# Kernel optimization log

Hardware: AMD Instinct MI355X
Metric: run time of the kernel (lower is better)

Reference implementation:

```python
import jax, jax.numpy as jnp
import numpy as np

VOCAB = 100000
SEQ = 2048
NSYN = 4
D = 300      # embedding_size
H1 = 300     # biLSTM output dim (150 per direction)
U = 150      # LSTM units per direction


def _lstm(x, Wk, Wr, b, reverse=False):
    """Keras-style LSTM over [S, D] -> [S, U]. Gate order i, f, g(cell), o."""
    if reverse:
        x = x[::-1]
    u = Wr.shape[0]

    def step(carry, xt):
        h, c = carry
        z = xt @ Wk + h @ Wr + b              # [4U]
        i, f, g, o = jnp.split(z, 4, axis=-1)
        i = jax.nn.sigmoid(i)
        f = jax.nn.sigmoid(f)
        g = jnp.tanh(g)
        o = jax.nn.sigmoid(o)
        c = f * c + i * g
        h = o * jnp.tanh(c)
        return (h, c), h

    init = (jnp.zeros((u,), x.dtype), jnp.zeros((u,), x.dtype))
    _, hs = jax.lax.scan(step, init, x)
    return hs[::-1] if reverse else hs


def setup_inputs() -> dict:
    key = jax.random.key(0)
    ks = jax.random.split(key, 14)
    w = 0.05  # small init so exp() attention coefficients stay stable
    return {
        "sentence": jax.random.randint(ks[0], (SEQ,), 0, VOCAB),
        "synonym_indices": jax.random.randint(ks[1], (VOCAB, NSYN), 0, VOCAB),
        "embedding_matrix": jax.random.normal(ks[2], (VOCAB, D), jnp.float32) * 0.1,
        # forward LSTM
        "Wk_f": jax.random.normal(ks[3], (D, 4 * U), jnp.float32) * w,
        "Wr_f": jax.random.normal(ks[4], (U, 4 * U), jnp.float32) * w,
        "b_f": jnp.zeros((4 * U,), jnp.float32),
        # backward LSTM
        "Wk_b": jax.random.normal(ks[5], (D, 4 * U), jnp.float32) * w,
        "Wr_b": jax.random.normal(ks[6], (U, 4 * U), jnp.float32) * w,
        "b_b": jnp.zeros((4 * U,), jnp.float32),
        # primary attention dense (h1 -> h1)
        "W1": jax.random.normal(ks[7], (H1, H1), jnp.float32) * w,
        "b1": jnp.zeros((H1,), jnp.float32),
        # secondary attention dense (h1 -> 1, tanh)
        "W2": jax.random.normal(ks[8], (H1, 1), jnp.float32) * w,
        "b2": jnp.zeros((1,), jnp.float32),
        # output heads
        "We": jax.random.normal(ks[9], (H1, 8), jnp.float32) * w,
        "be": jnp.zeros((8,), jnp.float32),
        "Ws": jax.random.normal(ks[10], (H1, 1), jnp.float32) * w,
        "bs": jnp.zeros((1,), jnp.float32),
    }


def reference(sentence, synonym_indices, embedding_matrix,
              Wk_f, Wr_f, b_f, Wk_b, Wr_b, b_b,
              W1, b1, W2, b2, We, be, Ws, bs):
    emb = embedding_matrix[sentence]                       # [S, D]
    hf = _lstm(emb, Wk_f, Wr_f, b_f)                       # [S, U]
    hb = _lstm(emb, Wk_b, Wr_b, b_b, reverse=True)         # [S, U]
    hidden = jnp.concatenate([hf, hb], axis=-1)            # [S, H1]

    # ---- primary attention (vectorized over all tokens) ----
    out = hidden @ W1 + b1                                 # [S, H1]
    S = sentence.shape[0]
    # Faithful off-by-one from the original loop: token 0 uses row 0,
    # token i (i>=1) uses out/hidden row i-1.
    idx = jnp.concatenate([jnp.zeros((1,), jnp.int32),
                           jnp.arange(S - 1, dtype=jnp.int32)])
    syn_emb = embedding_matrix[synonym_indices[sentence]]  # [S, NSYN, D]
    coeff = jnp.exp(jnp.einsum('skd,sd->sk', syn_emb, out[idx]))  # [S, NSYN]
    m = jnp.einsum('sk,skd->sd', coeff, syn_emb)           # [S, D]
    h_hats = m + hidden[idx]                               # [S, H1]

    # ---- secondary attention ----
    c2 = jnp.exp(jnp.tanh(h_hats @ W2 + b2))               # [S, 1]
    H = jnp.sum(c2 * h_hats, axis=0)[None, :]              # [1, H1]

    emotion_logits = H @ We + be                           # [1, 8]
    sentiment_logits = H @ Ws + bs                         # [1, 1]
    return (emotion_logits, sentiment_logits)
```

## Files before the change

### kernel.cpp

```cpp
#include <hip/hip_runtime.h>
#include <hip/hip_bf16.h>

#define SEQ   2048
#define DIM   300
#define UU    150
#define G4    600
#define H1    300
#define NSYN  4

typedef _Float16 half2v __attribute__((ext_vector_type(2)));
union HU { unsigned u; half2v h; };

static __device__ __forceinline__ float sigm(float x) { return 1.0f / (1.0f + __expf(-x)); }
static __device__ __forceinline__ float tanh_fast(float x) { return 1.0f - 2.0f / (1.0f + __expf(2.0f * x)); }

static __device__ __forceinline__ float dot2acc(unsigned w, int h, float acc) {
    asm("v_dot2_f32_f16 %0, %1, %2, %0" : "+v"(acc) : "v"(w), "s"(h));
    return acc;
}

#define LDS_BARRIER() asm volatile("s_waitcnt lgkmcnt(0)\n\ts_barrier" ::: "memory")

__global__ void xpre_kernel(const int* __restrict__ sentence,
                            const float* __restrict__ emb_mat,
                            const float* __restrict__ Wk_f,
                            const float* __restrict__ b_f,
                            const float* __restrict__ Wk_b,
                            const float* __restrict__ b_b,
                            float* __restrict__ Xf, float* __restrict__ Xb)
{
    const int dir = blockIdx.y;
    const float* Wk = dir ? Wk_b : Wk_f;
    const float* bb = dir ? b_b : b_f;
    float* X = dir ? Xb : Xf;

    const int s0  = blockIdx.x * 8;
    const int tid = threadIdx.x;

    __shared__ int   sids[8];
    __shared__ float embs[8][DIM];

    if (tid < 8) sids[tid] = sentence[s0 + tid];
    __syncthreads();
    for (int e = tid; e < 8 * DIM; e += 640) {
        int r = e / DIM, d = e - r * DIM;
        embs[r][d] = emb_mat[(long)sids[r] * DIM + d];
    }
    __syncthreads();

    if (tid < G4) {
        float acc[8];
        float bv = bb[tid];
        #pragma unroll
        for (int r = 0; r < 8; ++r) acc[r] = bv;
        for (int k = 0; k < DIM; ++k) {
            float wv = Wk[k * G4 + tid];
            #pragma unroll
            for (int r = 0; r < 8; ++r) acc[r] = fmaf(embs[r][k], wv, acc[r]);
        }
        #pragma unroll
        for (int r = 0; r < 8; ++r) X[(long)(s0 + r) * G4 + tid] = acc[r];
    }
}

#define REP75(F) \
  F(0) F(1) F(2) F(3) F(4) F(5) F(6) F(7) F(8) F(9) \
  F(10) F(11) F(12) F(13) F(14) F(15) F(16) F(17) F(18) F(19) \
  F(20) F(21) F(22) F(23) F(24) F(25) F(26) F(27) F(28) F(29) \
  F(30) F(31) F(32) F(33) F(34) F(35) F(36) F(37) F(38) F(39) \
  F(40) F(41) F(42) F(43) F(44) F(45) F(46) F(47) F(48) F(49) \
  F(50) F(51) F(52) F(53) F(54) F(55) F(56) F(57) F(58) F(59) \
  F(60) F(61) F(62) F(63) F(64) F(65) F(66) F(67) F(68) F(69) \
  F(70) F(71) F(72) F(73) F(74)

static __device__ __forceinline__ unsigned packpair(const float* __restrict__ Wr, int c, int k) {
    HU x;
    x.h.x = (_Float16)Wr[(2 * k) * G4 + c];
    x.h.y = (_Float16)Wr[(2 * k + 1) * G4 + c];
    return x.u;
}

__global__ __launch_bounds__(256) __attribute__((amdgpu_waves_per_eu(1, 1)))
void lstm_scan_kernel(
    const float* __restrict__ Xf, const float* __restrict__ Xb,
    const float* __restrict__ Wr_f, const float* __restrict__ Wr_b,
    float* __restrict__ hidden)
{
    const int dir = blockIdx.x;
    const float* X  = dir ? Xb : Xf;
    const float* Wr = dir ? Wr_b : Wr_f;
    const int tid  = threadIdx.x;
    const int lane = tid & 63;

    __shared__ float zs[G4];
    __shared__ __align__(4) _Float16 hs16[256];

    const int c0 = tid;
    const int c1 = tid + 256;
    const bool has2 = (tid < 88);
    const int c2 = has2 ? (tid + 512) : 599;

#define WDECL(k) unsigned wA_##k, wB_##k, wC_##k;
    REP75(WDECL)
#undef WDECL
#define WLOAD(k) wA_##k = packpair(Wr, c0, k); wB_##k = packpair(Wr, c1, k); wC_##k = packpair(Wr, c2, k);
    REP75(WLOAD)
#undef WLOAD

    if (tid < 128) ((unsigned*)hs16)[tid] = 0u;
    float c = 0.0f;

    int t = dir ? (SEQ - 1) : 0;
    const int dt = dir ? -1 : 1;
    float x0 = X[t * G4 + c0];
    float x1 = X[t * G4 + c1];
    float x2 = X[t * G4 + c2];
    __syncthreads();

    const unsigned* hp = (const unsigned*)hs16;

    for (int step = 0; step < SEQ; ++step) {
        const int tn = (step < SEQ - 1) ? (t + dt) : t;
        float xn0 = X[tn * G4 + c0];
        float xn1 = X[tn * G4 + c1];
        float xn2 = X[tn * G4 + c2];

        unsigned hr0 = hp[lane];
        unsigned hr1 = hp[64 + lane];

        float a0 = x0, a1 = x1, a2 = x2;
#define DOT(k) { int hk = ((k) < 64) ? __builtin_amdgcn_readlane((int)hr0, (k)) \
                                     : __builtin_amdgcn_readlane((int)hr1, (k) - 64); \
                 a0 = dot2acc(wA_##k, hk, a0); \
                 a1 = dot2acc(wB_##k, hk, a1); \
                 a2 = dot2acc(wC_##k, hk, a2); }
        REP75(DOT)
#undef DOT

        zs[c0] = a0;
        zs[c1] = a1;
        if (has2) zs[c2] = a2;
        LDS_BARRIER();

        if (tid < UU) {
            float zi = zs[tid], zf = zs[UU + tid], zg = zs[2 * UU + tid], zo = zs[3 * UU + tid];
            float ig = sigm(zi);
            float fg = sigm(zf);
            float gg = tanh_fast(zg);
            float og = sigm(zo);
            c = fg * c + ig * gg;
            float hv = og * tanh_fast(c);
            hs16[tid] = (_Float16)hv;
            hidden[(long)t * H1 + dir * UU + tid] = hv;
        }
        LDS_BARRIER();

        x0 = xn0; x1 = xn1; x2 = xn2;
        t = tn;
    }
}

__global__ void w1_kernel(const float* __restrict__ hidden,
                          const float* __restrict__ W1,
                          const float* __restrict__ b1,
                          float* __restrict__ outm)
{
    const int s0  = blockIdx.x * 8;
    const int tid = threadIdx.x;
    __shared__ float hl[8][H1];
    for (int e = tid; e < 8 * H1; e += 320)
        hl[e / H1][e - (e / H1) * H1] = hidden[(long)s0 * H1 + e];
    __syncthreads();

    if (tid < H1) {
        float acc[8];
        float bv = b1[tid];
        #pragma unroll
        for (int r = 0; r < 8; ++r) acc[r] = bv;
        for (int k = 0; k < H1; ++k) {
            float wv = W1[k * H1 + tid];
            #pragma unroll
            for (int r = 0; r < 8; ++r) acc[r] = fmaf(hl[r][k], wv, acc[r]);
        }
        #pragma unroll
        for (int r = 0; r < 8; ++r) outm[(long)(s0 + r) * H1 + tid] = acc[r];
    }
}

static __device__ __forceinline__ float4 blockReduce4(float4 v, float* red, int tid)
{
    #pragma unroll
    for (int off = 32; off > 0; off >>= 1) {
        v.x += __shfl_down(v.x, off);
        v.y += __shfl_down(v.y, off);
        v.z += __shfl_down(v.z, off);
        v.w += __shfl_down(v.w, off);
    }
    __syncthreads();
    if ((tid & 63) == 0) {
        int wv = tid >> 6;
        red[wv * 4 + 0] = v.x; red[wv * 4 + 1] = v.y;
        red[wv * 4 + 2] = v.z; red[wv * 4 + 3] = v.w;
    }
    __syncthreads();
    float4 r;
    r.x = red[0]; r.y = red[1]; r.z = red[2]; r.w = red[3];
    #pragma unroll
    for (int wv = 1; wv < 5; ++wv) {
        r.x += red[wv * 4 + 0]; r.y += red[wv * 4 + 1];
        r.z += red[wv * 4 + 2]; r.w += red[wv * 4 + 3];
    }
    return r;
}

static __device__ __forceinline__ float blockReduce1(float v, float* red, int tid)
{
    #pragma unroll
    for (int off = 32; off > 0; off >>= 1) v += __shfl_down(v, off);
    __syncthreads();
    if ((tid & 63) == 0) red[tid >> 6] = v;
    __syncthreads();
    return red[0] + red[1] + red[2] + red[3] + red[4];
}

__global__ void attn_kernel(const int* __restrict__ sentence,
                            const int* __restrict__ syn_idx,
                            const float* __restrict__ emb_mat,
                            const float* __restrict__ outm,
                            const float* __restrict__ hidden,
                            const float* __restrict__ W2,
                            const float* __restrict__ b2,
                            float* __restrict__ whh)
{
    const int s   = blockIdx.x;
    const int t   = s ? (s - 1) : 0;
    const int tid = threadIdx.x;
    __shared__ float red[20];

    const int sent = sentence[s];
    const long i0 = (long)syn_idx[sent * NSYN + 0] * DIM;
    const long i1 = (long)syn_idx[sent * NSYN + 1] * DIM;
    const long i2 = (long)syn_idx[sent * NSYN + 2] * DIM;
    const long i3 = (long)syn_idx[sent * NSYN + 3] * DIM;

    float se0 = 0.f, se1 = 0.f, se2 = 0.f, se3 = 0.f, od = 0.f, hd = 0.f;
    if (tid < DIM) {
        se0 = emb_mat[i0 + tid];
        se1 = emb_mat[i1 + tid];
        se2 = emb_mat[i2 + tid];
        se3 = emb_mat[i3 + tid];
        od  = outm[(long)t * H1 + tid];
        hd  = hidden[(long)t * H1 + tid];
    }

    float4 dots = blockReduce4(make_float4(se0 * od, se1 * od, se2 * od, se3 * od), red, tid);
    float c0 = __expf(dots.x), c1 = __expf(dots.y), c2c = __expf(dots.z), c3 = __expf(dots.w);

    float hh = fmaf(c0, se0, fmaf(c1, se1, fmaf(c2c, se2, fmaf(c3, se3, hd))));

    float w2v = (tid < DIM) ? W2[tid] : 0.f;
    float dot2 = blockReduce1(hh * w2v, red, tid);
    float cc = __expf(tanh_fast(dot2 + b2[0]));

    if (tid < DIM) whh[(long)s * H1 + tid] = cc * hh;
}

__global__ void hred_kernel(const float* __restrict__ whh, float* __restrict__ H)
{
    const int d   = blockIdx.x;
    const int tid = threadIdx.x;
    float acc = 0.f;
    for (int s = tid; s < SEQ; s += 256) acc += whh[(long)s * H1 + d];
    #pragma unroll
    for (int off = 32; off > 0; off >>= 1) acc += __shfl_down(acc, off);
    __shared__ float red[4];
    if ((tid & 63) == 0) red[tid >> 6] = acc;
    __syncthreads();
    if (tid == 0) H[d] = red[0] + red[1] + red[2] + red[3];
}

__global__ void logits_kernel(const float* __restrict__ H,
                              const float* __restrict__ We,
                              const float* __restrict__ be,
                              const float* __restrict__ Ws,
                              const float* __restrict__ bs,
                              float* __restrict__ outp)
{
    const int e = threadIdx.x;
    if (e < 9) {
        float acc = (e < 8) ? be[e] : bs[0];
        for (int d = 0; d < H1; ++d) {
            float wv = (e < 8) ? We[d * 8 + e] : Ws[d];
            acc = fmaf(H[d], wv, acc);
        }
        outp[e] = acc;
    }
}

extern "C" void kernel_launch(void* const* d_in, const int* in_sizes, int n_in,
                              void* d_out, int out_size, void* d_ws, size_t ws_size,
                              hipStream_t stream)
{
    const int* sentence   = (const int*)d_in[0];
    const int* syn_idx    = (const int*)d_in[1];
    const float* emb      = (const float*)d_in[2];
    const float* Wk_f     = (const float*)d_in[3];
    const float* Wr_f     = (const float*)d_in[4];
    const float* b_f      = (const float*)d_in[5];
    const float* Wk_b     = (const float*)d_in[6];
    const float* Wr_b     = (const float*)d_in[7];
    const float* b_b      = (const float*)d_in[8];
    const float* W1       = (const float*)d_in[9];
    const float* b1       = (const float*)d_in[10];
    const float* W2       = (const float*)d_in[11];
    const float* b2       = (const float*)d_in[12];
    const float* We       = (const float*)d_in[13];
    const float* be       = (const float*)d_in[14];
    const float* Ws       = (const float*)d_in[15];
    const float* bs       = (const float*)d_in[16];

    float* ws     = (float*)d_ws;
    float* Xf     = ws;
    float* Xb     = Xf + (long)SEQ * G4;
    float* hidden = Xb + (long)SEQ * G4;
    float* outm   = hidden + (long)SEQ * H1;
    float* whh    = outm + (long)SEQ * H1;
    float* H      = whh + (long)SEQ * H1;

    float* outp = (float*)d_out;

    xpre_kernel<<<dim3(SEQ / 8, 2), 640, 0, stream>>>(sentence, emb, Wk_f, b_f, Wk_b, b_b, Xf, Xb);
    lstm_scan_kernel<<<2, 256, 0, stream>>>(Xf, Xb, Wr_f, Wr_b, hidden);
    w1_kernel<<<SEQ / 8, 320, 0, stream>>>(hidden, W1, b1, outm);
    attn_kernel<<<SEQ, 320, 0, stream>>>(sentence, syn_idx, emb, outm, hidden, W2, b2, whh);
    hred_kernel<<<H1, 256, 0, stream>>>(whh, H);
    logits_kernel<<<1, 64, 0, stream>>>(H, We, be, Ws, bs, outp);
}
```

Before: 2.281 ms.

## Restructure LSTM scan so each lane owns two gates and exchanges via shuffle

The recurrent scan now maps each unit to a pair of lanes in different half-waves. One lane holds the i and g gate columns and the other holds f and o, and the i*g product is passed across with a cross-lane xor shuffle. This removes the LDS round trip of the full gate vector and one of the two barriers per timestep. The previous hidden state is read from a double-buffered LDS array with 128-bit vector loads, replacing scalar readlane broadcasts, and dot-product accumulation is split across two chains for more ILP. The block grows to 320 threads and drops the one-wave-per-EU attribute, so register pressure and occupancy behavior change.

Result: slower. 2.501 ms (+9.6%).

```diff
diff --git a/kernel.cpp b/kernel.cpp
--- a/kernel.cpp
+++ b/kernel.cpp
@@ -9,13 +9,14 @@
 #define NSYN  4
 
 typedef _Float16 half2v __attribute__((ext_vector_type(2)));
+typedef unsigned u32x4 __attribute__((ext_vector_type(4)));
 union HU { unsigned u; half2v h; };
 
 static __device__ __forceinline__ float sigm(float x) { return 1.0f / (1.0f + __expf(-x)); }
 static __device__ __forceinline__ float tanh_fast(float x) { return 1.0f - 2.0f / (1.0f + __expf(2.0f * x)); }
 
-static __device__ __forceinline__ float dot2acc(unsigned w, int h, float acc) {
-    asm("v_dot2_f32_f16 %0, %1, %2, %0" : "+v"(acc) : "v"(w), "s"(h));
+static __device__ __forceinline__ float dot2v(unsigned w, unsigned h, float acc) {
+    asm("v_dot2_f32_f16 %0, %1, %2, %0" : "+v"(acc) : "v"(w), "v"(h));
     return acc;
 }
 
@@ -63,7 +64,7 @@
     }
 }
 
-#define REP75(F) \
+#define REP76(F) \
   F(0) F(1) F(2) F(3) F(4) F(5) F(6) F(7) F(8) F(9) \
   F(10) F(11) F(12) F(13) F(14) F(15) F(16) F(17) F(18) F(19) \
   F(20) F(21) F(22) F(23) F(24) F(25) F(26) F(27) F(28) F(29) \
@@ -71,16 +72,17 @@
   F(40) F(41) F(42) F(43) F(44) F(45) F(46) F(47) F(48) F(49) \
   F(50) F(51) F(52) F(53) F(54) F(55) F(56) F(57) F(58) F(59) \
   F(60) F(61) F(62) F(63) F(64) F(65) F(66) F(67) F(68) F(69) \
-  F(70) F(71) F(72) F(73) F(74)
-
-static __device__ __forceinline__ unsigned packpair(const float* __restrict__ Wr, int c, int k) {
+  F(70) F(71) F(72) F(73) F(74) F(75)
+
+static __device__ __forceinline__ unsigned packpair2(const float* __restrict__ Wr, int c, int k) {
+    if (k >= 75) return 0u;
     HU x;
     x.h.x = (_Float16)Wr[(2 * k) * G4 + c];
     x.h.y = (_Float16)Wr[(2 * k + 1) * G4 + c];
     return x.u;
 }
 
-__global__ __launch_bounds__(256) __attribute__((amdgpu_waves_per_eu(1, 1)))
+__global__ __launch_bounds__(320)
 void lstm_scan_kernel(
     const float* __restrict__ Xf, const float* __restrict__ Xb,
     const float* __restrict__ Wr_f, const float* __restrict__ Wr_b,
@@ -90,73 +92,82 @@
     const float* X  = dir ? Xb : Xf;
     const float* Wr = dir ? Wr_b : Wr_f;
     const int tid  = threadIdx.x;
-    const int lane = tid & 63;
-
-    __shared__ float zs[G4];
-    __shared__ __align__(4) _Float16 hs16[256];
-
-    const int c0 = tid;
-    const int c1 = tid + 256;
-    const bool has2 = (tid < 88);
-    const int c2 = has2 ? (tid + 512) : 599;
-
-#define WDECL(k) unsigned wA_##k, wB_##k, wC_##k;
-    REP75(WDECL)
+    const int l    = tid & 63;
+    const int w    = tid >> 6;
+    const int isB  = l >> 5;
+    const int j    = (w << 5) + (l & 31);
+    const bool active = (j < UU);
+    const int u    = active ? j : (UU - 1);
+    const int cA   = u + isB * UU;
+    const int cB   = cA + 300;
+
+    __shared__ __align__(16) unsigned hsbuf[2][80];
+
+#define WDECL(k) unsigned wA_##k, wB_##k;
+    REP76(WDECL)
 #undef WDECL
-#define WLOAD(k) wA_##k = packpair(Wr, c0, k); wB_##k = packpair(Wr, c1, k); wC_##k = packpair(Wr, c2, k);
-    REP75(WLOAD)
+#define WLOAD(k) wA_##k = packpair2(Wr, cA, k); wB_##k = packpair2(Wr, cB, k);
+    REP76(WLOAD)
 #undef WLOAD
 
-    if (tid < 128) ((unsigned*)hs16)[tid] = 0u;
+    for (int e = tid; e < 160; e += 320) ((unsigned*)hsbuf)[e] = 0u;
+
     float c = 0.0f;
-
-    int t = dir ? (SEQ - 1) : 0;
+    int tt = dir ? (SEQ - 1) : 0;
     const int dt = dir ? -1 : 1;
-    float x0 = X[t * G4 + c0];
-    float x1 = X[t * G4 + c1];
-    float x2 = X[t * G4 + c2];
-    __syncthreads();
-
-    const unsigned* hp = (const unsigned*)hs16;
+    float xA = X[(long)tt * G4 + cA];
+    float xB = X[(long)tt * G4 + cB];
+    float* hout = hidden + dir * UU + u;
+    __syncthreads();
 
     for (int step = 0; step < SEQ; ++step) {
-        const int tn = (step < SEQ - 1) ? (t + dt) : t;
-        float xn0 = X[tn * G4 + c0];
-        float xn1 = X[tn * G4 + c1];
-        float xn2 = X[tn * G4 + c2];
-
-        unsigned hr0 = hp[lane];
-        unsigned hr1 = hp[64 + lane];
-
-        float a0 = x0, a1 = x1, a2 = x2;
-#define DOT(k) { int hk = ((k) < 64) ? __builtin_amdgcn_readlane((int)hr0, (k)) \
-                                     : __builtin_amdgcn_readlane((int)hr1, (k) - 64); \
-                 a0 = dot2acc(wA_##k, hk, a0); \
-                 a1 = dot2acc(wB_##k, hk, a1); \
-                 a2 = dot2acc(wC_##k, hk, a2); }
-        REP75(DOT)
-#undef DOT
-
-        zs[c0] = a0;
-        zs[c1] = a1;
-        if (has2) zs[c2] = a2;
-        LDS_BARRIER();
-
-        if (tid < UU) {
-            float zi = zs[tid], zf = zs[UU + tid], zg = zs[2 * UU + tid], zo = zs[3 * UU + tid];
-            float ig = sigm(zi);
-            float fg = sigm(zf);
-            float gg = tanh_fast(zg);
-            float og = sigm(zo);
-            c = fg * c + ig * gg;
-            float hv = og * tanh_fast(c);
-            hs16[tid] = (_Float16)hv;
-            hidden[(long)t * H1 + dir * UU + tid] = hv;
+        const int tn = (step < SEQ - 1) ? (tt + dt) : tt;
+        float xAn = X[(long)tn * G4 + cA];
+        float xBn = X[(long)tn * G4 + cB];
+
+        const u32x4* hb = (const u32x4*)hsbuf[step & 1];
+        u32x4 h0 = hb[0], h1 = hb[1], h2 = hb[2], h3 = hb[3], h4 = hb[4];
+        u32x4 h5 = hb[5], h6 = hb[6], h7 = hb[7], h8 = hb[8], h9 = hb[9];
+
+        float a0a = xA, a0b = 0.0f, a1a = xB, a1b = 0.0f;
+
+#define DOTQ(k0,k1,k2,k3,hv) \
+        a0a = dot2v(wA_##k0, hv.x, a0a); a1a = dot2v(wB_##k0, hv.x, a1a); \
+        a0b = dot2v(wA_##k1, hv.y, a0b); a1b = dot2v(wB_##k1, hv.y, a1b); \
+        a0a = dot2v(wA_##k2, hv.z, a0a); a1a = dot2v(wB_##k2, hv.z, a1a); \
+        a0b = dot2v(wA_##k3, hv.w, a0b); a1b = dot2v(wB_##k3, hv.w, a1b);
+
+        DOTQ(0,1,2,3,h0)     DOTQ(4,5,6,7,h1)     DOTQ(8,9,10,11,h2)
+        DOTQ(12,13,14,15,h3) DOTQ(16,17,18,19,h4)
+        h0 = hb[10]; h1 = hb[11]; h2 = hb[12]; h3 = hb[13]; h4 = hb[14];
+        DOTQ(20,21,22,23,h5) DOTQ(24,25,26,27,h6) DOTQ(28,29,30,31,h7)
+        DOTQ(32,33,34,35,h8) DOTQ(36,37,38,39,h9)
+        h5 = hb[15]; h6 = hb[16]; h7 = hb[17]; h8 = hb[18];
+        DOTQ(40,41,42,43,h0) DOTQ(44,45,46,47,h1) DOTQ(48,49,50,51,h2)
+        DOTQ(52,53,54,55,h3) DOTQ(56,57,58,59,h4)
+        DOTQ(60,61,62,63,h5) DOTQ(64,65,66,67,h6) DOTQ(68,69,70,71,h7)
+        DOTQ(72,73,74,75,h8)
+#undef DOTQ
+
+        const float a0 = a0a + a0b;
+        const float a1 = a1a + a1b;
+
+        float s0 = sigm(a0);
+        float t1 = tanh_fast(a1);
+        float s1 = sigm(a1);
+        float ig = s0 * t1;
+        float igx = __shfl_xor(ig, 32);
+        c = s0 * c + igx;
+        float th = tanh_fast(c);
+        float hv = s1 * th;
+
+        if (isB && active) {
+            ((_Float16*)hsbuf[(step & 1) ^ 1])[u] = (_Float16)hv;
+            hout[(long)tt * H1] = hv;
         }
         LDS_BARRIER();
 
-        x0 = xn0; x1 = xn1; x2 = xn2;
-        t = tn;
+        xA = xAn; xB = xBn; tt = tn;
     }
 }
 
@@ -330,7 +341,7 @@
     float* outp = (float*)d_out;
 
     xpre_kernel<<<dim3(SEQ / 8, 2), 640, 0, stream>>>(sentence, emb, Wk_f, b_f, Wk_b, b_b, Xf, Xb);
-    lstm_scan_kernel<<<2, 256, 0, stream>>>(Xf, Xb, Wr_f, Wr_b, hidden);
+    lstm_scan_kernel<<<2, 320, 0, stream>>>(Xf, Xb, Wr_f, Wr_b, hidden);
     w1_kernel<<<SEQ / 8, 320, 0, stream>>>(hidden, W1, b1, outm);
     attn_kernel<<<SEQ, 320, 0, stream>>>(sentence, syn_idx, emb, outm, hidden, W2, b2, whh);
     hred_kernel<<<H1, 256, 0, stream>>>(whh, H);
```
